# Kernel optimization log

Measured on AMD Instinct MI355X. Metric: run time of the kernel, lower is better.

## Reference

```python
import jax, jax.numpy as jnp
import numpy as np
from jax import lax


def _unfold(x, k, s):
    # torch.nn.functional.unfold: [B,C,H,W] -> [B, C*k*k, L], channel-major, row-major kernel offsets
    B, C, H, W = x.shape
    Ho = (H - k) // s + 1
    Wo = (W - k) // s + 1
    patches = [x[:, :, i:i + s * Ho:s, j:j + s * Wo:s] for i in range(k) for j in range(k)]
    stacked = jnp.stack(patches, axis=2)  # [B, C, k*k, Ho, Wo]
    return stacked.reshape(B, C * k * k, Ho * Wo)


def setup_inputs() -> dict:
    key = jax.random.key(0)
    x = jax.random.normal(key, (32, 69, 128, 128), dtype=jnp.float32)
    return {"x": x, "k": 2, "stride": 2}


def reference(x, k, stride):
    B, C, H, W = x.shape
    cs = C - 5  # number of pooled 'shape' channels
    # max pool over the first C-5 channels (kernel k, stride, no padding)
    pooled = lax.reduce_window(x[:, :cs], -jnp.inf, lax.max,
                               (1, 1, k, k), (1, 1, stride, stride), 'VALID')
    Ho, Wo = pooled.shape[2], pooled.shape[3]
    L = Ho * Wo
    kk = k * k
    # per-pixel L1 norm over channels, scaled
    shape_weights = jnp.sum(jnp.abs(x), axis=1, keepdims=True) / np.float32(np.sqrt(cs))
    sw = _unfold(shape_weights, k, stride)  # [B, kk, L]
    query = (sw / jnp.sum(jnp.abs(sw), axis=1, keepdims=True))[:, None]  # [B,1,kk,L]
    u_mean = _unfold(x[:, cs:cs + 2], k, stride).reshape(B, 2, kk, L)
    means = jnp.sum(u_mean * query, axis=2)  # [B,2,L]
    var1 = jnp.sum(_unfold(x[:, cs + 2:cs + 4], k, stride).reshape(B, 2, kk, L) * query, axis=2)
    var2 = jnp.sum((u_mean - means[:, :, None, :]) ** 2 * query, axis=2)
    window_var = var1 + var2
    cov1 = jnp.sum(_unfold(x[:, cs + 4:cs + 5], k, stride).reshape(B, 1, kk, L) * query, axis=2)
    cov2 = jnp.sum((u_mean[:, 0:1] - means[:, 0:1, None, :])
                   * (u_mean[:, 1:2] - means[:, 1:2, None, :])
                   * query ** 2, axis=2)
    window_covar = cov1 + cov2
    # cat + fold with (1,1) kernel == reshape to [B,5,Ho,Wo]
    agg = jnp.concatenate([means, window_var, window_covar], axis=1).reshape(B, 5, Ho, Wo)
    return jnp.concatenate([pooled, agg], axis=1)
```

## Files before the change

kernel.cpp:

```cpp
#include <hip/hip_runtime.h>

#define B_ 32
#define C_ 69
#define CS_ 64
#define H_ 128
#define W_ 128
#define HO_ 64
#define WO_ 64

__global__ __launch_bounds__(256) void spatial_pool_kernel(
        const float* __restrict__ x, float* __restrict__ out) {
    int t = blockIdx.x * blockDim.x + threadIdx.x;
    int wo = t & (WO_ - 1);
    int ho = (t >> 6) & (HO_ - 1);
    int b  = t >> 12;

    const float* xb = x + (size_t)b * C_ * H_ * W_;
    float*       ob = out + (size_t)b * C_ * HO_ * WO_;

    const int h0 = 2 * ho, w0 = 2 * wo;
    const size_t base0 = (size_t)h0 * W_ + w0;
    const size_t base1 = base0 + W_;
    const size_t ostride = (size_t)HO_ * WO_;
    const size_t opix = (size_t)ho * WO_ + wo;

    float S0 = 0.f, S1 = 0.f, S2 = 0.f, S3 = 0.f;

    #pragma unroll 8
    for (int c = 0; c < CS_; ++c) {
        const float* xc = xb + (size_t)c * (H_ * W_);
        float2 r0 = *(const float2*)(xc + base0);
        float2 r1 = *(const float2*)(xc + base1);
        S0 += fabsf(r0.x); S1 += fabsf(r0.y);
        S2 += fabsf(r1.x); S3 += fabsf(r1.y);
        float m = fmaxf(fmaxf(r0.x, r0.y), fmaxf(r1.x, r1.y));
        ob[(size_t)c * ostride + opix] = m;
    }

    float sp[5][4];
    #pragma unroll
    for (int d = 0; d < 5; ++d) {
        const float* xc = xb + (size_t)(CS_ + d) * (H_ * W_);
        float2 r0 = *(const float2*)(xc + base0);
        float2 r1 = *(const float2*)(xc + base1);
        sp[d][0] = r0.x; sp[d][1] = r0.y; sp[d][2] = r1.x; sp[d][3] = r1.y;
        S0 += fabsf(r0.x); S1 += fabsf(r0.y);
        S2 += fabsf(r1.x); S3 += fabsf(r1.y);
    }

    float inv = 1.0f / (S0 + S1 + S2 + S3);
    float q[4] = {S0 * inv, S1 * inv, S2 * inv, S3 * inv};

    float m0 = 0.f, m1 = 0.f;
    #pragma unroll
    for (int j = 0; j < 4; ++j) {
        m0 += sp[0][j] * q[j];
        m1 += sp[1][j] * q[j];
    }

    float v0 = 0.f, v1 = 0.f, cv = 0.f;
    #pragma unroll
    for (int j = 0; j < 4; ++j) {
        float d0 = sp[0][j] - m0;
        float d1 = sp[1][j] - m1;
        v0 += sp[2][j] * q[j] + d0 * d0 * q[j];
        v1 += sp[3][j] * q[j] + d1 * d1 * q[j];
        cv += sp[4][j] * q[j] + d0 * d1 * q[j] * q[j];
    }

    ob[(size_t)(CS_ + 0) * ostride + opix] = m0;
    ob[(size_t)(CS_ + 1) * ostride + opix] = m1;
    ob[(size_t)(CS_ + 2) * ostride + opix] = v0;
    ob[(size_t)(CS_ + 3) * ostride + opix] = v1;
    ob[(size_t)(CS_ + 4) * ostride + opix] = cv;
}

extern "C" void kernel_launch(void* const* d_in, const int* in_sizes, int n_in,
                              void* d_out, int out_size, void* d_ws, size_t ws_size,
                              hipStream_t stream) {
    const float* x = (const float*)d_in[0];
    float* out = (float*)d_out;
    const int total = B_ * HO_ * WO_;
    const int block = 256;
    const int grid = (total + block - 1) / block;
    spatial_pool_kernel<<<grid, block, 0, stream>>>(x, out);
}
```

Before: 215.5 us.

## Split channel loop across four waves per output row with shared-memory reduction

Each block now handles one output row of one batch, and its four waves each process a quarter of the channels for the same 64 pixels. Per-pixel absolute sums are reduced through shared memory, and the tail channels are staged in shared memory for the final weighted statistics, computed by one wave. This shortens each thread's serial channel loop to raise memory-level parallelism. It adds a block barrier and leaves three waves idle during the final step.

```diff
diff --git a/kernel.cpp b/kernel.cpp
--- a/kernel.cpp
+++ b/kernel.cpp
@@ -7,72 +7,106 @@
 #define W_ 128
 #define HO_ 64
 #define WO_ 64
+#define HW_ (H_ * W_)
+#define OHW_ (HO_ * WO_)
 
-__global__ __launch_bounds__(256) void spatial_pool_kernel(
+__global__ __launch_bounds__(256, 8) void spatial_pool_kernel(
         const float* __restrict__ x, float* __restrict__ out) {
-    int t = blockIdx.x * blockDim.x + threadIdx.x;
-    int wo = t & (WO_ - 1);
-    int ho = (t >> 6) & (HO_ - 1);
-    int b  = t >> 12;
+    __shared__ float part[4][4][64];
+    __shared__ float tail[5][4][64];
 
-    const float* xb = x + (size_t)b * C_ * H_ * W_;
-    float*       ob = out + (size_t)b * C_ * HO_ * WO_;
+    const int lane = threadIdx.x & 63;
+    const int w    = threadIdx.x >> 6;
+    const int blk  = blockIdx.x;
+    const int ho   = blk & 63;
+    const int b    = blk >> 6;
 
-    const int h0 = 2 * ho, w0 = 2 * wo;
-    const size_t base0 = (size_t)h0 * W_ + w0;
-    const size_t base1 = base0 + W_;
-    const size_t ostride = (size_t)HO_ * WO_;
-    const size_t opix = (size_t)ho * WO_ + wo;
+    const float* xb = x   + (size_t)b * (C_ * HW_);
+    float*       ob = out + (size_t)b * (C_ * OHW_);
+
+    const int base0 = (2 * ho) * W_ + 2 * lane;
+    const int base1 = base0 + W_;
+    const int opix  = ho * WO_ + lane;
 
     float S0 = 0.f, S1 = 0.f, S2 = 0.f, S3 = 0.f;
 
-    #pragma unroll 8
-    for (int c = 0; c < CS_; ++c) {
-        const float* xc = xb + (size_t)c * (H_ * W_);
+    const int cbeg = w * 17;
+    const int cend_pooled = (w == 3) ? CS_ : (cbeg + 17);
+
+    #pragma unroll 4
+    for (int c = cbeg; c < cend_pooled; ++c) {
+        const float* xc = xb + c * HW_;
         float2 r0 = *(const float2*)(xc + base0);
         float2 r1 = *(const float2*)(xc + base1);
         S0 += fabsf(r0.x); S1 += fabsf(r0.y);
         S2 += fabsf(r1.x); S3 += fabsf(r1.y);
         float m = fmaxf(fmaxf(r0.x, r0.y), fmaxf(r1.x, r1.y));
-        ob[(size_t)c * ostride + opix] = m;
+        ob[c * OHW_ + opix] = m;
     }
 
-    float sp[5][4];
-    #pragma unroll
-    for (int d = 0; d < 5; ++d) {
-        const float* xc = xb + (size_t)(CS_ + d) * (H_ * W_);
-        float2 r0 = *(const float2*)(xc + base0);
-        float2 r1 = *(const float2*)(xc + base1);
-        sp[d][0] = r0.x; sp[d][1] = r0.y; sp[d][2] = r1.x; sp[d][3] = r1.y;
-        S0 += fabsf(r0.x); S1 += fabsf(r0.y);
-        S2 += fabsf(r1.x); S3 += fabsf(r1.y);
+    if (w == 3) {
+        #pragma unroll
+        for (int d = 0; d < 5; ++d) {
+            const float* xc = xb + (CS_ + d) * HW_;
+            float2 r0 = *(const float2*)(xc + base0);
+            float2 r1 = *(const float2*)(xc + base1);
+            tail[d][0][lane] = r0.x; tail[d][1][lane] = r0.y;
+            tail[d][2][lane] = r1.x; tail[d][3][lane] = r1.y;
+            S0 += fabsf(r0.x); S1 += fabsf(r0.y);
+            S2 += fabsf(r1.x); S3 += fabsf(r1.y);
+        }
     }
 
-    float inv = 1.0f / (S0 + S1 + S2 + S3);
-    float q[4] = {S0 * inv, S1 * inv, S2 * inv, S3 * inv};
+    part[w][0][lane] = S0; part[w][1][lane] = S1;
+    part[w][2][lane] = S2; part[w][3][lane] = S3;
+    __syncthreads();
 
-    float m0 = 0.f, m1 = 0.f;
-    #pragma unroll
-    for (int j = 0; j < 4; ++j) {
-        m0 += sp[0][j] * q[j];
-        m1 += sp[1][j] * q[j];
+    if (w == 0) {
+        float q[4];
+        float tot = 0.f;
+        #pragma unroll
+        for (int j = 0; j < 4; ++j) {
+            q[j] = part[0][j][lane] + part[1][j][lane]
+                 + part[2][j][lane] + part[3][j][lane];
+            tot += q[j];
+        }
+        float inv = 1.0f / tot;
+        #pragma unroll
+        for (int j = 0; j < 4; ++j) q[j] *= inv;
+
+        float sp0[4], sp1[4], sp2[4], sp3[4], sp4[4];
+        #pragma unroll
+        for (int j = 0; j < 4; ++j) {
+            sp0[j] = tail[0][j][lane];
+            sp1[j] = tail[1][j][lane];
+            sp2[j] = tail[2][j][lane];
+            sp3[j] = tail[3][j][lane];
+            sp4[j] = tail[4][j][lane];
+        }
+
+        float m0 = 0.f, m1 = 0.f;
+        #pragma unroll
+        for (int j = 0; j < 4; ++j) {
+            m0 += sp0[j] * q[j];
+            m1 += sp1[j] * q[j];
+        }
+
+        float v0 = 0.f, v1 = 0.f, cv = 0.f;
+        #pragma unroll
+        for (int j = 0; j < 4; ++j) {
+            float d0 = sp0[j] - m0;
+            float d1 = sp1[j] - m1;
+            v0 += sp2[j] * q[j] + d0 * d0 * q[j];
+            v1 += sp3[j] * q[j] + d1 * d1 * q[j];
+            cv += sp4[j] * q[j] + d0 * d1 * q[j] * q[j];
+        }
+
+        ob[(CS_ + 0) * OHW_ + opix] = m0;
+        ob[(CS_ + 1) * OHW_ + opix] = m1;
+        ob[(CS_ + 2) * OHW_ + opix] = v0;
+        ob[(CS_ + 3) * OHW_ + opix] = v1;
+        ob[(CS_ + 4) * OHW_ + opix] = cv;
     }
-
-    float v0 = 0.f, v1 = 0.f, cv = 0.f;
-    #pragma unroll
-    for (int j = 0; j < 4; ++j) {
-        float d0 = sp[0][j] - m0;
-        float d1 = sp[1][j] - m1;
-        v0 += sp[2][j] * q[j] + d0 * d0 * q[j];
-        v1 += sp[3][j] * q[j] + d1 * d1 * q[j];
-        cv += sp[4][j] * q[j] + d0 * d1 * q[j] * q[j];
-    }
-
-    ob[(size_t)(CS_ + 0) * ostride + opix] = m0;
-    ob[(size_t)(CS_ + 1) * ostride + opix] = m1;
-    ob[(size_t)(CS_ + 2) * ostride + opix] = v0;
-    ob[(size_t)(CS_ + 3) * ostride + opix] = v1;
-    ob[(size_t)(CS_ + 4) * ostride + opix] = cv;
 }
 
 extern "C" void kernel_launch(void* const* d_in, const int* in_sizes, int n_in,
@@ -80,8 +114,6 @@
                               hipStream_t stream) {
     const float* x = (const float*)d_in[0];
     float* out = (float*)d_out;
-    const int total = B_ * HO_ * WO_;
-    const int block = 256;
-    const int grid = (total + block - 1) / block;
-    spatial_pool_kernel<<<grid, block, 0, stream>>>(x, out);
+    const int grid = B_ * HO_;
+    spatial_pool_kernel<<<grid, 256, 0, stream>>>(x, out);
 }
```

Result: no change. 215.3 us (-0.1%).
